# Performance work log

Hardware: AMD Instinct MI355X
Metric: run time of the kernel (lower is better)

## Reference

```python
import jax, jax.numpy as jnp
import numpy as np

V = 1_000_000
NODE_DIM = 128
HIDDEN = 128
OUT_DIM = 128
GLOBAL_DIM = 64
N_GRAPH = 50_000


def setup_inputs() -> dict:
    key = jax.random.key(0)
    ks = jax.random.split(key, 10)
    s1 = 1.0 / np.sqrt(NODE_DIM)
    s3 = 1.0 / np.sqrt(2 * HIDDEN + GLOBAL_DIM)
    return {
        "x": jax.random.normal(ks[0], (V, NODE_DIM), dtype=jnp.float32),
        "node2graph": jax.random.randint(ks[1], (V,), 0, N_GRAPH, dtype=jnp.int64),
        "global_x": jax.random.normal(ks[2], (N_GRAPH, GLOBAL_DIM), dtype=jnp.float32),
        "W1": jax.random.uniform(ks[3], (HIDDEN, NODE_DIM), jnp.float32, -s1, s1),
        "b1": jax.random.uniform(ks[4], (HIDDEN,), jnp.float32, -s1, s1),
        "W2": jax.random.uniform(ks[5], (HIDDEN, NODE_DIM), jnp.float32, -s1, s1),
        "b2": jax.random.uniform(ks[6], (HIDDEN,), jnp.float32, -s1, s1),
        "W3": jax.random.uniform(ks[7], (OUT_DIM, 2 * HIDDEN + GLOBAL_DIM), jnp.float32, -s3, s3),
        "b3": jax.random.uniform(ks[8], (OUT_DIM,), jnp.float32, -s3, s3),
    }


def reference(x, node2graph, global_x, W1, b1, W2, b2, W3, b3):
    # gated projection: linear1(x) * sigmoid(linear2(x))   [V, H]
    h = (x @ W1.T + b1) * jax.nn.sigmoid(x @ W2.T + b2)
    # segment sum / mean over graphs   [N, H]
    Z1 = jax.ops.segment_sum(h, node2graph, num_segments=N_GRAPH)
    counts = jax.ops.segment_sum(jnp.ones((h.shape[0],), h.dtype), node2graph,
                                 num_segments=N_GRAPH)
    Z2 = Z1 / jnp.maximum(counts, 1.0)[:, None]
    Z = jnp.concatenate([Z1, Z2, global_x], axis=-1)  # [N, 2H+Fg]
    return jax.nn.relu(Z @ W3.T + b3)  # [N, OUT_DIM]
```

## Files before the change

kernel.cpp:

```cpp
#include <hip/hip_runtime.h>
#include <cmath>

#define V_NODES  1000000
#define NODE_DIM 128
#define HIDDEN   128
#define OUT_DIM  128
#define GDIM     64
#define NGRAPH   50000

typedef unsigned short u16;
typedef __attribute__((ext_vector_type(8))) short          short8;
typedef __attribute__((ext_vector_type(8))) unsigned short ushort8;
typedef __attribute__((ext_vector_type(8))) __bf16         bf16x8;
typedef __attribute__((ext_vector_type(4))) float          f32x4;

__device__ __forceinline__ u16 f2bf(float f) {
  unsigned u = __builtin_bit_cast(unsigned, f);
  u += 0x7fff + ((u >> 16) & 1);
  return (u16)(u >> 16);
}

__device__ __forceinline__ f32x4 mfma_bf16(bf16x8 a, bf16x8 b, f32x4 c) {
  return __builtin_amdgcn_mfma_f32_16x16x32_bf16(a, b, c, 0, 0, 0);
}

__global__ __launch_bounds__(256) void convert_weights(
    const float* __restrict__ W1, const float* __restrict__ W2,
    const float* __restrict__ W3,
    u16* __restrict__ w1b, u16* __restrict__ w2b, u16* __restrict__ w3b) {
  int i = blockIdx.x * 256 + threadIdx.x;
  if (i < NODE_DIM * HIDDEN) {
    w1b[i] = f2bf(W1[i]);
    w2b[i] = f2bf(W2[i]);
  }
  if (i < OUT_DIM * (2 * HIDDEN + GDIM)) w3b[i] = f2bf(W3[i]);
}

__global__ __launch_bounds__(256, 2) void gated_scatter(
    const float* __restrict__ x, const int* __restrict__ n2g,
    const u16* __restrict__ w1b, const u16* __restrict__ w2b,
    const float* __restrict__ b1, const float* __restrict__ b2,
    float* __restrict__ Z1, float* __restrict__ cnt) {
  extern __shared__ u16 lds[];
  u16* sW1 = lds;
  u16* sW2 = lds + 16384;
  const int tid = threadIdx.x;

#pragma unroll
  for (int i = 0; i < 8; ++i) {
    int m = i * 256 + tid;
    int n = m >> 4, c = m & 15;
    int p = c ^ (n & 15);
    *(ushort8*)(sW1 + n * 128 + p * 8) = *(const ushort8*)(w1b + m * 8);
    *(ushort8*)(sW2 + n * 128 + p * 8) = *(const ushort8*)(w2b + m * 8);
  }
  __syncthreads();

  const int lane = tid & 63;
  const int wv   = tid >> 6;
  const int q    = lane >> 4;
  const int mr   = lane & 15;
  const int rowbase = blockIdx.x * 64 + wv * 16;
  const int arow    = rowbase + mr;

  f32x4 acc1[8] = {};
  f32x4 acc2[8] = {};

#pragma unroll
  for (int kc = 0; kc < 4; ++kc) {
    const int k0 = kc * 32;
    const float* ap = x + (size_t)arow * NODE_DIM + k0 + q * 8;
    float4 a0 = *(const float4*)ap;
    float4 a1 = *(const float4*)(ap + 4);
    bf16x8 af;
    af[0] = (__bf16)a0.x; af[1] = (__bf16)a0.y; af[2] = (__bf16)a0.z; af[3] = (__bf16)a0.w;
    af[4] = (__bf16)a1.x; af[5] = (__bf16)a1.y; af[6] = (__bf16)a1.z; af[7] = (__bf16)a1.w;

    const int p = ((k0 >> 3) + q) ^ mr;
#pragma unroll
    for (int t = 0; t < 8; ++t) {
      const int n = t * 16 + mr;
      short8 bs1 = *(const short8*)(sW1 + n * 128 + p * 8);
      short8 bs2 = *(const short8*)(sW2 + n * 128 + p * 8);
      acc1[t] = mfma_bf16(af, __builtin_bit_cast(bf16x8, bs1), acc1[t]);
      acc2[t] = mfma_bf16(af, __builtin_bit_cast(bf16x8, bs2), acc2[t]);
    }
  }

  int g[4];
#pragma unroll
  for (int r = 0; r < 4; ++r) g[r] = n2g[rowbase + q * 4 + r];

#pragma unroll
  for (int t = 0; t < 8; ++t) {
    const int col = t * 16 + mr;
    const float bb1 = b1[col];
    const float bb2 = b2[col];
#pragma unroll
    for (int r = 0; r < 4; ++r) {
      float l1 = acc1[t][r] + bb1;
      float l2 = acc2[t][r] + bb2;
      float h  = l1 / (1.0f + __expf(-l2));
      atomicAdd(Z1 + (size_t)g[r] * HIDDEN + col, h);
    }
  }

  if (tid < 64) atomicAdd(cnt + n2g[blockIdx.x * 64 + tid], 1.0f);
}

__global__ __launch_bounds__(256, 4) void readout_k(
    const float* __restrict__ Z1, const float* __restrict__ cnt,
    const float* __restrict__ gx, const u16* __restrict__ w3b,
    const float* __restrict__ b3, float* __restrict__ out) {
  const int tid  = threadIdx.x;
  const int lane = tid & 63;
  const int wv   = tid >> 6;
  const int q    = lane >> 4;
  const int mr   = lane & 15;
  const int rowbase = blockIdx.x * 64 + wv * 16;
  const int arow    = rowbase + mr;
  const bool rowok  = arow < NGRAPH;

  float inv = 0.0f;
  if (rowok) inv = 1.0f / fmaxf(cnt[arow], 1.0f);

  f32x4 acc[8] = {};

#pragma unroll
  for (int kc = 0; kc < 10; ++kc) {
    const int k0 = kc * 32;
    float av[8];
    if (rowok) {
      if (k0 < 128) {
        const float* p = Z1 + (size_t)arow * HIDDEN + k0 + q * 8;
        float4 a0 = *(const float4*)p;
        float4 a1 = *(const float4*)(p + 4);
        av[0]=a0.x; av[1]=a0.y; av[2]=a0.z; av[3]=a0.w;
        av[4]=a1.x; av[5]=a1.y; av[6]=a1.z; av[7]=a1.w;
      } else if (k0 < 256) {
        const float* p = Z1 + (size_t)arow * HIDDEN + (k0 - 128) + q * 8;
        float4 a0 = *(const float4*)p;
        float4 a1 = *(const float4*)(p + 4);
        av[0]=a0.x*inv; av[1]=a0.y*inv; av[2]=a0.z*inv; av[3]=a0.w*inv;
        av[4]=a1.x*inv; av[5]=a1.y*inv; av[6]=a1.z*inv; av[7]=a1.w*inv;
      } else {
        const float* p = gx + (size_t)arow * GDIM + (k0 - 256) + q * 8;
        float4 a0 = *(const float4*)p;
        float4 a1 = *(const float4*)(p + 4);
        av[0]=a0.x; av[1]=a0.y; av[2]=a0.z; av[3]=a0.w;
        av[4]=a1.x; av[5]=a1.y; av[6]=a1.z; av[7]=a1.w;
      }
    } else {
#pragma unroll
      for (int j = 0; j < 8; ++j) av[j] = 0.0f;
    }
    bf16x8 af;
#pragma unroll
    for (int j = 0; j < 8; ++j) af[j] = (__bf16)av[j];

#pragma unroll
    for (int t = 0; t < 8; ++t) {
      const int n = t * 16 + mr;
      short8 bs = *(const short8*)(w3b + (size_t)n * (2 * HIDDEN + GDIM) + k0 + q * 8);
      acc[t] = mfma_bf16(af, __builtin_bit_cast(bf16x8, bs), acc[t]);
    }
  }

#pragma unroll
  for (int t = 0; t < 8; ++t) {
    const int col = t * 16 + mr;
    const float bb = b3[col];
#pragma unroll
    for (int r = 0; r < 4; ++r) {
      const int row = rowbase + q * 4 + r;
      if (row < NGRAPH)
        out[(size_t)row * OUT_DIM + col] = fmaxf(acc[t][r] + bb, 0.0f);
    }
  }
}

extern "C" void kernel_launch(void* const* d_in, const int* in_sizes, int n_in,
                              void* d_out, int out_size, void* d_ws, size_t ws_size,
                              hipStream_t stream) {
  const float* x   = (const float*)d_in[0];
  const int*   n2g = (const int*)d_in[1];
  const float* gx  = (const float*)d_in[2];
  const float* W1  = (const float*)d_in[3];
  const float* b1  = (const float*)d_in[4];
  const float* W2  = (const float*)d_in[5];
  const float* b2  = (const float*)d_in[6];
  const float* W3  = (const float*)d_in[7];
  const float* b3  = (const float*)d_in[8];
  float* out = (float*)d_out;

  char* ws = (char*)d_ws;
  u16*   w1b = (u16*)(ws);
  u16*   w2b = (u16*)(ws + 32768);
  u16*   w3b = (u16*)(ws + 65536);
  float* Z1  = (float*)(ws + 147456);
  float* cnt = (float*)(ws + 147456 + (size_t)NGRAPH * HIDDEN * 4);

  hipMemsetAsync(ws + 147456, 0,
                 (size_t)NGRAPH * HIDDEN * 4 + (size_t)NGRAPH * 4, stream);

  convert_weights<<<160, 256, 0, stream>>>(W1, W2, W3, w1b, w2b, w3b);

  gated_scatter<<<V_NODES / 64, 256, 2 * 16384 * sizeof(u16), stream>>>(
      x, n2g, w1b, w2b, b1, b2, Z1, cnt);

  readout_k<<<(NGRAPH + 63) / 64, 256, 0, stream>>>(Z1, cnt, gx, w3b, b3, out);
}
```

Measured before the change: 1.078 ms.

## Sort nodes by graph via counting sort and pre-reduce segments before atomics

Adds a counting-sort pipeline (integer count, single-block scan, atomic scatter) that orders node indices by graph id. The gated GEMM kernel then gathers x rows in sorted order and sums consecutive same-graph rows within each lane and across quad lanes with shuffles, issuing one atomic per segment run instead of one per row. This is meant to cut global float atomic traffic, which averages about 20 nodes per graph. The cost is three extra kernels, a serial single-block scan, and gathered rather than contiguous reads of x, which hurts coalescing.

After: 1.180 ms. 9.4% more time.

```diff
diff --git a/kernel.cpp b/kernel.cpp
--- a/kernel.cpp
+++ b/kernel.cpp
@@ -36,11 +36,60 @@
   if (i < OUT_DIM * (2 * HIDDEN + GDIM)) w3b[i] = f2bf(W3[i]);
 }
 
-__global__ __launch_bounds__(256, 2) void gated_scatter(
-    const float* __restrict__ x, const int* __restrict__ n2g,
+__global__ __launch_bounds__(256) void count_k(
+    const int* __restrict__ n2g, int* __restrict__ cnt) {
+  int i = blockIdx.x * 256 + threadIdx.x;
+  if (i < V_NODES) atomicAdd(&cnt[n2g[i]], 1);
+}
+
+__global__ __launch_bounds__(1024) void scan_k(
+    const int* __restrict__ cnt, int* __restrict__ head) {
+  __shared__ int ls[1024];
+  const int t = threadIdx.x;
+  const int base = t * 49;
+  int s = 0;
+#pragma unroll 7
+  for (int j = 0; j < 49; ++j) {
+    int idx = base + j;
+    if (idx < NGRAPH) s += cnt[idx];
+  }
+  ls[t] = s;
+  __syncthreads();
+  for (int d = 1; d < 1024; d <<= 1) {
+    int v = (t >= d) ? ls[t - d] : 0;
+    __syncthreads();
+    ls[t] += v;
+    __syncthreads();
+  }
+  int run = ls[t] - s;
+#pragma unroll 7
+  for (int j = 0; j < 49; ++j) {
+    int idx = base + j;
+    if (idx < NGRAPH) {
+      head[idx] = run;
+      run += cnt[idx];
+    }
+  }
+}
+
+__global__ __launch_bounds__(256) void scatter_k(
+    const int* __restrict__ n2g, int* __restrict__ head,
+    int* __restrict__ ord, u16* __restrict__ gs) {
+  int i = blockIdx.x * 256 + threadIdx.x;
+  if (i < V_NODES) {
+    int g = n2g[i];
+    int pos = atomicAdd(&head[g], 1);
+    ord[pos] = i;
+    gs[pos] = (u16)g;
+  }
+}
+
+__global__ __launch_bounds__(256, 2) void gather_gated(
+    const float* __restrict__ x, const int* __restrict__ ord,
+    const u16* __restrict__ gs,
     const u16* __restrict__ w1b, const u16* __restrict__ w2b,
     const float* __restrict__ b1, const float* __restrict__ b2,
-    float* __restrict__ Z1, float* __restrict__ cnt) {
+    float* __restrict__ Z1) {
   extern __shared__ u16 lds[];
   u16* sW1 = lds;
   u16* sW2 = lds + 16384;
@@ -61,7 +110,7 @@
   const int q    = lane >> 4;
   const int mr   = lane & 15;
   const int rowbase = blockIdx.x * 64 + wv * 16;
-  const int arow    = rowbase + mr;
+  const int node    = ord[rowbase + mr];
 
   f32x4 acc1[8] = {};
   f32x4 acc2[8] = {};
@@ -69,7 +118,7 @@
 #pragma unroll
   for (int kc = 0; kc < 4; ++kc) {
     const int k0 = kc * 32;
-    const float* ap = x + (size_t)arow * NODE_DIM + k0 + q * 8;
+    const float* ap = x + (size_t)node * NODE_DIM + k0 + q * 8;
     float4 a0 = *(const float4*)ap;
     float4 a1 = *(const float4*)(ap + 4);
     bf16x8 af;
@@ -87,29 +136,54 @@
     }
   }
 
-  int g[4];
-#pragma unroll
-  for (int r = 0; r < 4; ++r) g[r] = n2g[rowbase + q * 4 + r];
+  const int rb4 = rowbase + q * 4;
+  const int gq0 = gs[rb4 + 0];
+  const int gq1 = gs[rb4 + 1];
+  const int gq2 = gs[rb4 + 2];
+  const int gq3 = gs[rb4 + 3];
+  const int gprev = (q > 0) ? (int)gs[rb4 - 1] : -1;
+  const int gnext = (q < 3) ? (int)gs[rb4 + 4] : -1;
+
+  const int uni_own  = (gq0 == gq1) & (gq1 == gq2) & (gq2 == gq3);
+  const int conn_own = (gq0 == gprev) ? 1 : 0;
+  const int conn_p   = __shfl_up(conn_own, 16, 64);
+  const int uni_p    = __shfl_up(uni_own, 16, 64);
+  const int conn_p2  = __shfl_up(conn_own, 32, 64);
+  const int uni_p2   = __shfl_up(uni_own, 32, 64);
+  const bool c1 = conn_own != 0;
+  const bool c2 = c1 && (uni_p  && conn_p);
+  const bool c3 = c2 && (uni_p2 && conn_p2);
 
 #pragma unroll
   for (int t = 0; t < 8; ++t) {
     const int col = t * 16 + mr;
     const float bb1 = b1[col];
     const float bb2 = b2[col];
-#pragma unroll
-    for (int r = 0; r < 4; ++r) {
-      float l1 = acc1[t][r] + bb1;
-      float l2 = acc2[t][r] + bb2;
-      float h  = l1 / (1.0f + __expf(-l2));
-      atomicAdd(Z1 + (size_t)g[r] * HIDDEN + col, h);
-    }
-  }
-
-  if (tid < 64) atomicAdd(cnt + n2g[blockIdx.x * 64 + tid], 1.0f);
+
+    float l1, l2;
+    l1 = acc1[t][0] + bb1; l2 = acc2[t][0] + bb2; const float h0 = l1 / (1.0f + __expf(-l2));
+    l1 = acc1[t][1] + bb1; l2 = acc2[t][1] + bb2; const float h1 = l1 / (1.0f + __expf(-l2));
+    l1 = acc1[t][2] + bb1; l2 = acc2[t][2] + bb2; const float h2 = l1 / (1.0f + __expf(-l2));
+    l1 = acc1[t][3] + bb1; l2 = acc2[t][3] + bb2; const float h3 = l1 / (1.0f + __expf(-l2));
+
+    float ts = h3;
+    if (gq2 == gq3) { ts += h2; if (gq1 == gq3) { ts += h1; if (gq0 == gq3) ts += h0; } }
+    const float ts1 = __shfl_up(ts, 16, 64);
+    const float ts2 = __shfl_up(ts, 32, 64);
+    const float ts3 = __shfl_up(ts, 48, 64);
+    float carry = 0.0f;
+    if (c1) { carry = ts1; if (c2) { carry += ts2; if (c3) carry += ts3; } }
+
+    float run = carry + h0;
+    if (gq1 != gq0) { atomicAdd(Z1 + (size_t)gq0 * HIDDEN + col, run); run = h1; } else run += h1;
+    if (gq2 != gq1) { atomicAdd(Z1 + (size_t)gq1 * HIDDEN + col, run); run = h2; } else run += h2;
+    if (gq3 != gq2) { atomicAdd(Z1 + (size_t)gq2 * HIDDEN + col, run); run = h3; } else run += h3;
+    if (gnext != gq3) atomicAdd(Z1 + (size_t)gq3 * HIDDEN + col, run);
+  }
 }
 
 __global__ __launch_bounds__(256, 4) void readout_k(
-    const float* __restrict__ Z1, const float* __restrict__ cnt,
+    const float* __restrict__ Z1, const int* __restrict__ cnt,
     const float* __restrict__ gx, const u16* __restrict__ w3b,
     const float* __restrict__ b3, float* __restrict__ out) {
   const int tid  = threadIdx.x;
@@ -122,7 +196,7 @@
   const bool rowok  = arow < NGRAPH;
 
   float inv = 0.0f;
-  if (rowok) inv = 1.0f / fmaxf(cnt[arow], 1.0f);
+  if (rowok) inv = 1.0f / fmaxf((float)cnt[arow], 1.0f);
 
   f32x4 acc[8] = {};
 
@@ -194,19 +268,28 @@
   float* out = (float*)d_out;
 
   char* ws = (char*)d_ws;
-  u16*   w1b = (u16*)(ws);
-  u16*   w2b = (u16*)(ws + 32768);
-  u16*   w3b = (u16*)(ws + 65536);
-  float* Z1  = (float*)(ws + 147456);
-  float* cnt = (float*)(ws + 147456 + (size_t)NGRAPH * HIDDEN * 4);
+  u16*   w1b  = (u16*)(ws);
+  u16*   w2b  = (u16*)(ws + 32768);
+  u16*   w3b  = (u16*)(ws + 65536);
+  float* Z1   = (float*)(ws + 147456);
+  int*   cnt  = (int*)(ws + 147456 + (size_t)NGRAPH * HIDDEN * 4);
+  int*   head = (int*)(ws + 147456 + (size_t)NGRAPH * HIDDEN * 4 + (size_t)NGRAPH * 4);
+  int*   ord  = (int*)(ws + 147456 + (size_t)NGRAPH * HIDDEN * 4 + (size_t)NGRAPH * 8);
+  u16*   gs   = (u16*)(ws + 147456 + (size_t)NGRAPH * HIDDEN * 4 + (size_t)NGRAPH * 8
+                          + (size_t)V_NODES * 4);
 
   hipMemsetAsync(ws + 147456, 0,
                  (size_t)NGRAPH * HIDDEN * 4 + (size_t)NGRAPH * 4, stream);
 
   convert_weights<<<160, 256, 0, stream>>>(W1, W2, W3, w1b, w2b, w3b);
 
-  gated_scatter<<<V_NODES / 64, 256, 2 * 16384 * sizeof(u16), stream>>>(
-      x, n2g, w1b, w2b, b1, b2, Z1, cnt);
+  const int nb = (V_NODES + 255) / 256;
+  count_k<<<nb, 256, 0, stream>>>(n2g, cnt);
+  scan_k<<<1, 1024, 0, stream>>>(cnt, head);
+  scatter_k<<<nb, 256, 0, stream>>>(n2g, head, ord, gs);
+
+  gather_gated<<<V_NODES / 64, 256, 2 * 16384 * sizeof(u16), stream>>>(
+      x, ord, gs, w1b, w2b, b1, b2, Z1);
 
   readout_k<<<(NGRAPH + 63) / 64, 256, 0, stream>>>(Z1, cnt, gx, w3b, b3, out);
 }
```
